# Optimization experiments

Hardware: AMD Instinct MI355X
Metric: run time of the kernel (lower is better)

## Reference

```python
import jax, jax.numpy as jnp
import numpy as np

B = 1024
INPUT_SIZE = 2048
OUTPUT_SIZE = 2048
E = 131072  # number of sparse connections


def setup_inputs() -> dict:
    key = jax.random.key(0)
    k1, k2, k3, k4 = jax.random.split(key, 4)
    x = jax.random.normal(k1, (B, INPUT_SIZE), dtype=jnp.float32)
    weights = jax.random.normal(k2, (E,), dtype=jnp.float32)
    in_idx = jax.random.randint(k3, (E,), 0, INPUT_SIZE, dtype=jnp.int64)
    out_idx = jax.random.randint(k4, (E,), 0, OUTPUT_SIZE, dtype=jnp.int64)
    return {"x": x, "weights": weights, "in_idx": in_idx, "out_idx": out_idx}


def reference(x, weights, in_idx, out_idx):
    # Original: for (i, o), w in connections: output[:, o] += w * x[:, i]
    # Vectorized as a single gather-multiply-scatter (duplicates sum):
    contrib = x[:, in_idx] * weights[None, :]  # [B, E]
    out = jnp.zeros((x.shape[0], OUTPUT_SIZE), dtype=x.dtype)
    out = out.at[:, out_idx].add(contrib)  # scatter-add along output dim
    return out
```

## Files before the change

kernel.cpp:

```cpp
#include <hip/hip_runtime.h>
#include <hip/hip_bf16.h>

#define BATCH  1024
#define IN_SZ  2048
#define OUT_SZ 2048
#define E_N    131072

#define NT     256
#define R8     8
#define CGN    8
#define RGN    (BATCH / R8)
#define NSEG   2
#define SEG_D  64
#define K_MAX  (NSEG * SEG_D)
#define CPAD   16

__device__ __forceinline__ unsigned int bf16_rne(float f) {
    unsigned int u = __float_as_uint(f);
    return (u + 0x7FFFu + ((u >> 16) & 1u)) >> 16;
}

__global__ void fill_kernel(const int* __restrict__ iidx, const int* __restrict__ oidx,
                            const float* __restrict__ w,
                            int* __restrict__ cursor, unsigned int* __restrict__ ell) {
    const int e = blockIdx.x * 256 + threadIdx.x;
    const int o = oidx[e];
    const int i = iidx[e];
    const unsigned int wb = bf16_rne(w[e]) << 16;
    const int s = e >> 16;
    const int pos = atomicAdd(&cursor[(s * OUT_SZ + o) * CPAD], 1);
    if (pos < SEG_D)
        ell[(size_t)(s * SEG_D + pos) * OUT_SZ + o] = wb | (unsigned int)(i << 4);
}

__global__ __launch_bounds__(NT) void spmm_kernel(const float* __restrict__ x,
                                                  const unsigned int* __restrict__ ell,
                                                  const int* __restrict__ cursor,
                                                  float* __restrict__ out) {
    __shared__ __align__(16) unsigned short xsT[IN_SZ * R8];
    const int cgid = blockIdx.x;
    const int r0   = blockIdx.y * R8;
    const int tid  = threadIdx.x;

    const float* xb = x + (size_t)r0 * IN_SZ;
    #pragma unroll
    for (int it = 0; it < IN_SZ / NT; ++it) {
        const int c = it * NT + tid;
        unsigned int p[4];
        #pragma unroll
        for (int j = 0; j < 4; ++j) {
            const float lo = xb[(size_t)(2 * j) * IN_SZ + c];
            const float hi = xb[(size_t)(2 * j + 1) * IN_SZ + c];
            p[j] = (bf16_rne(hi) << 16) | bf16_rne(lo);
        }
        *(uint4*)&xsT[c * R8] = make_uint4(p[0], p[1], p[2], p[3]);
    }
    __syncthreads();

    const int c = cgid * NT + tid;
    float acc[R8];
    #pragma unroll
    for (int r = 0; r < R8; r++) acc[r] = 0.f;

    #pragma unroll
    for (int s = 0; s < NSEG; ++s) {
        int cnt = cursor[(s * OUT_SZ + c) * CPAD];
        cnt = cnt < SEG_D ? cnt : SEG_D;
        const unsigned int* ep = ell + (size_t)(s * SEG_D) * OUT_SZ + c;
        #pragma unroll 4
        for (int k = 0; k < cnt; ++k) {
            const unsigned int e = ep[(size_t)k * OUT_SZ];
            const float wv = __uint_as_float(e & 0xFFFF0000u);
            const uint4 xv = *(const uint4*)((const char*)xsT + (e & 0xFFFFu));
            acc[0] = fmaf(wv, __uint_as_float(xv.x << 16),         acc[0]);
            acc[1] = fmaf(wv, __uint_as_float(xv.x & 0xFFFF0000u), acc[1]);
            acc[2] = fmaf(wv, __uint_as_float(xv.y << 16),         acc[2]);
            acc[3] = fmaf(wv, __uint_as_float(xv.y & 0xFFFF0000u), acc[3]);
            acc[4] = fmaf(wv, __uint_as_float(xv.z << 16),         acc[4]);
            acc[5] = fmaf(wv, __uint_as_float(xv.z & 0xFFFF0000u), acc[5]);
            acc[6] = fmaf(wv, __uint_as_float(xv.w << 16),         acc[6]);
            acc[7] = fmaf(wv, __uint_as_float(xv.w & 0xFFFF0000u), acc[7]);
        }
    }

    float* op = out + (size_t)r0 * OUT_SZ + c;
    #pragma unroll
    for (int r = 0; r < R8; r++) op[(size_t)r * OUT_SZ] = acc[r];
}

__global__ __launch_bounds__(NT) void sparse_row_kernel(
    const float* __restrict__ x, const float* __restrict__ w,
    const int* __restrict__ iidx, const int* __restrict__ oidx,
    float* __restrict__ out) {
    __shared__ float xs[IN_SZ];
    __shared__ float acc[OUT_SZ];
    const int b = blockIdx.x, tid = threadIdx.x;
    const float4* xrow = (const float4*)(x + (size_t)b * IN_SZ);
    float4* xs4 = (float4*)xs;
    for (int t = tid; t < IN_SZ / 4; t += NT) xs4[t] = xrow[t];
    float4* acc4 = (float4*)acc;
    const float4 z = make_float4(0.f, 0.f, 0.f, 0.f);
    for (int t = tid; t < OUT_SZ / 4; t += NT) acc4[t] = z;
    __syncthreads();
    for (int e = tid; e < E_N; e += NT)
        atomicAdd(&acc[oidx[e]], w[e] * xs[iidx[e]]);
    __syncthreads();
    float4* orow = (float4*)(out + (size_t)b * OUT_SZ);
    for (int t = tid; t < OUT_SZ / 4; t += NT) orow[t] = acc4[t];
}

extern "C" void kernel_launch(void* const* d_in, const int* in_sizes, int n_in,
                              void* d_out, int out_size, void* d_ws, size_t ws_size,
                              hipStream_t stream) {
    const float* x    = (const float*)d_in[0];
    const float* wts  = (const float*)d_in[1];
    const int*   iidx = (const int*)d_in[2];
    const int*   oidx = (const int*)d_in[3];
    float* out = (float*)d_out;
    (void)in_sizes; (void)n_in; (void)out_size;

    const size_t cursor_bytes = (size_t)NSEG * OUT_SZ * CPAD * sizeof(int);
    const size_t need = cursor_bytes + (size_t)K_MAX * OUT_SZ * sizeof(unsigned int);
    if (ws_size < need) {
        sparse_row_kernel<<<BATCH, NT, 0, stream>>>(x, wts, iidx, oidx, out);
        return;
    }

    int* cursor = (int*)d_ws;
    unsigned int* ell = (unsigned int*)((char*)d_ws + cursor_bytes);

    hipMemsetAsync(cursor, 0, cursor_bytes, stream);
    fill_kernel<<<E_N / 256, 256, 0, stream>>>(iidx, oidx, wts, cursor, ell);
    dim3 grid(CGN, RGN);
    spmm_kernel<<<grid, NT, 0, stream>>>(x, ell, cursor, out);
}
```

Measured before the change: 99.03 us.

## Transpose x to bf16 column-major and make SpMM wave-uniform per output column

A new prep kernel transposes x into a global bf16 buffer (input feature major, batch contiguous) and also zeroes the cursor array, which replaces the memset. The ELL buffer becomes output-column major so each wave reads its column's entries with scalar readfirstlane loads. Each lane then covers 4 batch rows with coalesced 8-byte global loads instead of LDS-staged gathers. Results go through an LDS tile so they can be stored as float4. The change adds a global transposed copy of x and one extra pass over x, and drops the per-block LDS staging of x that was repeated across output column groups.

```diff
diff --git a/kernel.cpp b/kernel.cpp
--- a/kernel.cpp
+++ b/kernel.cpp
@@ -1,5 +1,4 @@
 #include <hip/hip_runtime.h>
-#include <hip/hip_bf16.h>
 
 #define BATCH  1024
 #define IN_SZ  2048
@@ -7,85 +6,115 @@
 #define E_N    131072
 
 #define NT     256
-#define R8     8
-#define CGN    8
-#define RGN    (BATCH / R8)
 #define NSEG   2
 #define SEG_D  64
 #define K_MAX  (NSEG * SEG_D)
 #define CPAD   16
+#define ZERO_BLKS 16
 
 __device__ __forceinline__ unsigned int bf16_rne(float f) {
     unsigned int u = __float_as_uint(f);
     return (u + 0x7FFFu + ((u >> 16) & 1u)) >> 16;
 }
 
-__global__ void fill_kernel(const int* __restrict__ iidx, const int* __restrict__ oidx,
-                            const float* __restrict__ w,
-                            int* __restrict__ cursor, unsigned int* __restrict__ ell) {
-    const int e = blockIdx.x * 256 + threadIdx.x;
-    const int o = oidx[e];
-    const int i = iidx[e];
-    const unsigned int wb = bf16_rne(w[e]) << 16;
-    const int s = e >> 16;
-    const int pos = atomicAdd(&cursor[(s * OUT_SZ + o) * CPAD], 1);
-    if (pos < SEG_D)
-        ell[(size_t)(s * SEG_D + pos) * OUT_SZ + o] = wb | (unsigned int)(i << 4);
+__global__ __launch_bounds__(NT) void prep1_kernel(const float* __restrict__ x,
+                                                   unsigned short* __restrict__ xt,
+                                                   int* __restrict__ cursor) {
+    __shared__ float lds[64][65];
+    const int tid = threadIdx.x;
+    const int b   = blockIdx.x;
+
+    if (b < ZERO_BLKS) {
+        int4* c4 = (int4*)cursor;
+        #pragma unroll
+        for (int k = 0; k < 4; ++k)
+            c4[b * 1024 + k * NT + tid] = make_int4(0, 0, 0, 0);
+    }
+
+    const int c0 = (b & 31) * 64;
+    const int r0 = (b >> 5) * 64;
+    #pragma unroll
+    for (int k = 0; k < 16; ++k) {
+        const int idx = k * NT + tid;
+        const int r = idx >> 6, cl = idx & 63;
+        lds[r][cl] = x[(size_t)(r0 + r) * IN_SZ + c0 + cl];
+    }
+    __syncthreads();
+    #pragma unroll
+    for (int k = 0; k < 8; ++k) {
+        const int idx = k * NT + tid;
+        const int cl = idx >> 5;
+        const int rp = (idx & 31) * 2;
+        const unsigned int v = bf16_rne(lds[rp][cl]) | (bf16_rne(lds[rp + 1][cl]) << 16);
+        *(unsigned int*)&xt[(size_t)(c0 + cl) * BATCH + r0 + rp] = v;
+    }
 }
 
-__global__ __launch_bounds__(NT) void spmm_kernel(const float* __restrict__ x,
-                                                  const unsigned int* __restrict__ ell,
-                                                  const int* __restrict__ cursor,
-                                                  float* __restrict__ out) {
-    __shared__ __align__(16) unsigned short xsT[IN_SZ * R8];
-    const int cgid = blockIdx.x;
-    const int r0   = blockIdx.y * R8;
+__global__ void fill_kernel(const int4* __restrict__ iidx4, const int4* __restrict__ oidx4,
+                            const float4* __restrict__ w4,
+                            int* __restrict__ cursor, unsigned int* __restrict__ ell) {
+    const int t = blockIdx.x * NT + threadIdx.x;
+    const int4   ii = iidx4[t];
+    const int4   oo = oidx4[t];
+    const float4 ww = w4[t];
+    const int ebase = t * 4;
+    #pragma unroll
+    for (int j = 0; j < 4; ++j) {
+        const int i = (&ii.x)[j];
+        const int o = (&oo.x)[j];
+        const unsigned int packed = (bf16_rne((&ww.x)[j]) << 16) | (unsigned int)i;
+        const int s = (ebase + j) >> 16;
+        const int pos = atomicAdd(&cursor[(s * OUT_SZ + o) * CPAD], 1);
+        if (pos < SEG_D)
+            ell[(size_t)o * K_MAX + s * SEG_D + pos] = packed;
+    }
+}
+
+__global__ __launch_bounds__(NT) void spmm2_kernel(const unsigned short* __restrict__ xt,
+                                                   const unsigned int* __restrict__ ell,
+                                                   const int* __restrict__ cursor,
+                                                   float* __restrict__ out) {
+    __shared__ float tile[256][9];
     const int tid  = threadIdx.x;
+    const int w    = tid >> 6;
+    const int lane = tid & 63;
+    const int c0   = blockIdx.x * 8;
+    const int r0   = blockIdx.y * 256;
+    const unsigned short* xtb = xt + r0 + lane * 4;
 
-    const float* xb = x + (size_t)r0 * IN_SZ;
     #pragma unroll
-    for (int it = 0; it < IN_SZ / NT; ++it) {
-        const int c = it * NT + tid;
-        unsigned int p[4];
+    for (int p = 0; p < 2; ++p) {
+        const int cs = __builtin_amdgcn_readfirstlane(c0 + w * 2 + p);
+        const unsigned int* ep = ell + (size_t)cs * K_MAX;
+        float a0 = 0.f, a1 = 0.f, a2 = 0.f, a3 = 0.f;
         #pragma unroll
-        for (int j = 0; j < 4; ++j) {
-            const float lo = xb[(size_t)(2 * j) * IN_SZ + c];
-            const float hi = xb[(size_t)(2 * j + 1) * IN_SZ + c];
-            p[j] = (bf16_rne(hi) << 16) | bf16_rne(lo);
+        for (int s = 0; s < NSEG; ++s) {
+            int cnt = cursor[(s * OUT_SZ + cs) * CPAD];
+            cnt = cnt < SEG_D ? cnt : SEG_D;
+            const unsigned int* p2 = ep + s * SEG_D;
+            #pragma unroll 4
+            for (int k = 0; k < cnt; ++k) {
+                const unsigned int e =
+                    (unsigned int)__builtin_amdgcn_readfirstlane((int)p2[k]);
+                const float wv = __uint_as_float(e & 0xFFFF0000u);
+                const uint2 xv = *(const uint2*)(xtb + ((e & 0x7FFu) << 10));
+                a0 = fmaf(wv, __uint_as_float(xv.x << 16),         a0);
+                a1 = fmaf(wv, __uint_as_float(xv.x & 0xFFFF0000u), a1);
+                a2 = fmaf(wv, __uint_as_float(xv.y << 16),         a2);
+                a3 = fmaf(wv, __uint_as_float(xv.y & 0xFFFF0000u), a3);
+            }
         }
-        *(uint4*)&xsT[c * R8] = make_uint4(p[0], p[1], p[2], p[3]);
+        const int cl = w * 2 + p;
+        tile[lane * 4 + 0][cl] = a0;
+        tile[lane * 4 + 1][cl] = a1;
+        tile[lane * 4 + 2][cl] = a2;
+        tile[lane * 4 + 3][cl] = a3;
     }
     __syncthreads();
 
-    const int c = cgid * NT + tid;
-    float acc[R8];
-    #pragma unroll
-    for (int r = 0; r < R8; r++) acc[r] = 0.f;
-
-    #pragma unroll
-    for (int s = 0; s < NSEG; ++s) {
-        int cnt = cursor[(s * OUT_SZ + c) * CPAD];
-        cnt = cnt < SEG_D ? cnt : SEG_D;
-        const unsigned int* ep = ell + (size_t)(s * SEG_D) * OUT_SZ + c;
-        #pragma unroll 4
-        for (int k = 0; k < cnt; ++k) {
-            const unsigned int e = ep[(size_t)k * OUT_SZ];
-            const float wv = __uint_as_float(e & 0xFFFF0000u);
-            const uint4 xv = *(const uint4*)((const char*)xsT + (e & 0xFFFFu));
-            acc[0] = fmaf(wv, __uint_as_float(xv.x << 16),         acc[0]);
-            acc[1] = fmaf(wv, __uint_as_float(xv.x & 0xFFFF0000u), acc[1]);
-            acc[2] = fmaf(wv, __uint_as_float(xv.y << 16),         acc[2]);
-            acc[3] = fmaf(wv, __uint_as_float(xv.y & 0xFFFF0000u), acc[3]);
-            acc[4] = fmaf(wv, __uint_as_float(xv.z << 16),         acc[4]);
-            acc[5] = fmaf(wv, __uint_as_float(xv.z & 0xFFFF0000u), acc[5]);
-            acc[6] = fmaf(wv, __uint_as_float(xv.w << 16),         acc[6]);
-            acc[7] = fmaf(wv, __uint_as_float(xv.w & 0xFFFF0000u), acc[7]);
-        }
-    }
-
-    float* op = out + (size_t)r0 * OUT_SZ + c;
-    #pragma unroll
-    for (int r = 0; r < R8; r++) op[(size_t)r * OUT_SZ] = acc[r];
+    float* op = out + (size_t)(r0 + tid) * OUT_SZ + c0;
+    *(float4*)op       = make_float4(tile[tid][0], tile[tid][1], tile[tid][2], tile[tid][3]);
+    *(float4*)(op + 4) = make_float4(tile[tid][4], tile[tid][5], tile[tid][6], tile[tid][7]);
 }
 
 __global__ __launch_bounds__(NT) void sparse_row_kernel(
@@ -120,17 +149,20 @@
     (void)in_sizes; (void)n_in; (void)out_size;
 
     const size_t cursor_bytes = (size_t)NSEG * OUT_SZ * CPAD * sizeof(int);
-    const size_t need = cursor_bytes + (size_t)K_MAX * OUT_SZ * sizeof(unsigned int);
-    if (ws_size < need) {
+    const size_t ell_bytes    = (size_t)OUT_SZ * K_MAX * sizeof(unsigned int);
+    const size_t xt_bytes     = (size_t)IN_SZ * BATCH * sizeof(unsigned short);
+    if (ws_size < cursor_bytes + ell_bytes + xt_bytes) {
         sparse_row_kernel<<<BATCH, NT, 0, stream>>>(x, wts, iidx, oidx, out);
         return;
     }
 
     int* cursor = (int*)d_ws;
-    unsigned int* ell = (unsigned int*)((char*)d_ws + cursor_bytes);
+    unsigned int*   ell = (unsigned int*)((char*)d_ws + cursor_bytes);
+    unsigned short* xt  = (unsigned short*)((char*)d_ws + cursor_bytes + ell_bytes);
 
-    hipMemsetAsync(cursor, 0, cursor_bytes, stream);
-    fill_kernel<<<E_N / 256, 256, 0, stream>>>(iidx, oidx, wts, cursor, ell);
-    dim3 grid(CGN, RGN);
-    spmm_kernel<<<grid, NT, 0, stream>>>(x, ell, cursor, out);
+    prep1_kernel<<<512, NT, 0, stream>>>(x, xt, cursor);
+    fill_kernel<<<E_N / 4 / NT, NT, 0, stream>>>((const int4*)iidx, (const int4*)oidx,
+                                                 (const float4*)wts, cursor, ell);
+    dim3 grid(OUT_SZ / 8, BATCH / 256);
+    spmm2_kernel<<<grid, NT, 0, stream>>>(xt, ell, cursor, out);
 }
```

Result: slower. 119.1 us (+20.2%).
